# Kernel tuning notes

Hardware: AMD Instinct MI355X
Metric: run time of the kernel (lower is better)

Reference implementation:

```python
import math
import jax, jax.numpy as jnp
import numpy as np

N_HEAD = 12
LN_EPS = 1e-5

def _gelu(x):
    # NewGELU: tanh approximation
    c = math.sqrt(2.0 / math.pi)
    return 0.5 * x * (1.0 + jnp.tanh(c * (x + 0.044715 * x ** 3)))

def _ln(x, w, b):
    m = x.mean(-1, keepdims=True)
    v = x.var(-1, keepdims=True)
    return (x - m) / jnp.sqrt(v + LN_EPS) * w + b

def setup_inputs() -> dict:
    key = jax.random.key(0)
    ks = jax.random.split(key, 8)
    L, C, V, BS = 12, 768, 30522, 1024
    B, T = 4, 1024
    std = 0.02
    inp = {
        'idx': jax.random.randint(ks[0], (B, T), 0, V),
        'wte': jax.random.normal(ks[1], (V, C), jnp.float32) * std,
        'wpe': jax.random.normal(ks[2], (BS, C), jnp.float32) * std,
        'ln1_w': jnp.ones((L, C), jnp.float32),
        'ln1_b': jnp.zeros((L, C), jnp.float32),
        'attn_w': jax.random.normal(ks[3], (L, 3 * C, C), jnp.float32) * std,
        'attn_b': jnp.zeros((L, 3 * C), jnp.float32),
        'proj_w': jax.random.normal(ks[4], (L, C, C), jnp.float32) * (std / math.sqrt(2 * L)),
        'proj_b': jnp.zeros((L, C), jnp.float32),
        'ln2_w': jnp.ones((L, C), jnp.float32),
        'ln2_b': jnp.zeros((L, C), jnp.float32),
        'fc_w': jax.random.normal(ks[5], (L, 4 * C, C), jnp.float32) * std,
        'fc_b': jnp.zeros((L, 4 * C), jnp.float32),
        'mproj_w': jax.random.normal(ks[6], (L, C, 4 * C), jnp.float32) * (std / math.sqrt(2 * L)),
        'mproj_b': jnp.zeros((L, C), jnp.float32),
        'lnf_w': jnp.ones((C,), jnp.float32),
        'lnf_b': jnp.zeros((C,), jnp.float32),
        'lm_head_w': jax.random.normal(ks[7], (V, C), jnp.float32) * std,
    }
    return inp

def reference(idx, wte, wpe, ln1_w, ln1_b, attn_w, attn_b, proj_w, proj_b,
              ln2_w, ln2_b, fc_w, fc_b, mproj_w, mproj_b, lnf_w, lnf_b, lm_head_w):
    B, T = idx.shape
    C = wte.shape[1]
    H = N_HEAD
    D = C // H
    scale = 1.0 / math.sqrt(D)
    x = wte[idx] + wpe[:T][None]  # [B,T,C], drop is identity (p=0)

    def block(x, p):
        l1w, l1b, aw, ab, pw, pb, l2w, l2b, fw, fb, mw, mb = p
        h = _ln(x, l1w, l1b)
        qkv = jnp.einsum('btc,ec->bte', h, aw) + ab  # [B,T,3C]
        q, k, v = jnp.split(qkv, 3, axis=-1)
        q = q.reshape(B, T, H, D)
        k = k.reshape(B, T, H, D)
        v = v.reshape(B, T, H, D)
        att = jnp.einsum('bthd,bshd->bhts', q, k) * scale  # [B,H,T,T]
        att = jax.nn.softmax(att, axis=-1)  # mask=None: full attention
        y = jnp.einsum('bhts,bshd->bthd', att, v).reshape(B, T, C)
        x = x + jnp.einsum('btc,oc->bto', y, pw) + pb
        h = _gelu(jnp.einsum('btc,fc->btf', _ln(x, l2w, l2b), fw) + fb)
        x = x + jnp.einsum('btf,cf->btc', h, mw) + mb
        return x, None

    x, _ = jax.lax.scan(block, x, (ln1_w, ln1_b, attn_w, attn_b, proj_w, proj_b,
                                   ln2_w, ln2_b, fc_w, fc_b, mproj_w, mproj_b))
    x = _ln(x, lnf_w, lnf_b)
    logits = jnp.einsum('btc,vc->btv', x, lm_head_w)  # [B,T,V]
    return logits
```

## Files before the change

### kernel.cpp

```cpp
#include <hip/hip_runtime.h>
#include <hip/hip_bf16.h>
#include <math.h>

typedef __attribute__((ext_vector_type(8))) short short8;
typedef __attribute__((ext_vector_type(4))) float f32x4;

typedef unsigned short u16;

__device__ __forceinline__ u16 f2bf(float f) {
    union { float f; unsigned int u; } v; v.f = f;
    unsigned int u = v.u;
    unsigned int r = (u + 0x7fffu + ((u >> 16) & 1u)) >> 16;
    return (u16)r;
}
__device__ __forceinline__ float bf2f(u16 u) {
    union { unsigned int u; float f; } v; v.u = ((unsigned int)u) << 16;
    return v.f;
}

__device__ __forceinline__ void gload16(const void* g, void* l) {
    __builtin_amdgcn_global_load_lds(
        (const __attribute__((address_space(1))) void*)g,
        (__attribute__((address_space(3))) void*)l, 16, 0, 0);
}

__global__ __launch_bounds__(256) void castw_kernel(const float* __restrict__ src,
                                                    u16* __restrict__ dst,
                                                    long n, long npad) {
    long i = ((long)blockIdx.x * 256 + threadIdx.x) * 4;
    const long stride = (long)gridDim.x * 1024;
    for (; i < npad; i += stride) {
        ushort4 o;
        if (i < n) {
            float4 v = *reinterpret_cast<const float4*>(src + i);
            o.x = f2bf(v.x); o.y = f2bf(v.y); o.z = f2bf(v.z); o.w = f2bf(v.w);
        } else {
            o = make_ushort4(0, 0, 0, 0);
        }
        *reinterpret_cast<ushort4*>(dst + i) = o;
    }
}

__global__ __launch_bounds__(256) void embed_kernel(const int* __restrict__ idx,
                                                    const float* __restrict__ wte,
                                                    const float* __restrict__ wpe,
                                                    float* __restrict__ x) {
    const int row = blockIdx.x;
    const int tid = threadIdx.x;
    const int t = row & 1023;
    const int tok = idx[row];
    const float* we = wte + (size_t)tok * 768;
    const float* pe = wpe + (size_t)t * 768;
    float* xr = x + (size_t)row * 768;
    xr[tid]       = we[tid]       + pe[tid];
    xr[tid + 256] = we[tid + 256] + pe[tid + 256];
    xr[tid + 512] = we[tid + 512] + pe[tid + 512];
}

__global__ __launch_bounds__(256) void ln_kernel(const float* __restrict__ x,
                                                 const float* __restrict__ w,
                                                 const float* __restrict__ b,
                                                 u16* __restrict__ out) {
    const int wid = threadIdx.x >> 6, lane = threadIdx.x & 63;
    const int row = blockIdx.x * 4 + wid;
    const float* xr = x + (size_t)row * 768;
    const float4 v0 = *reinterpret_cast<const float4*>(xr + lane * 4);
    const float4 v1 = *reinterpret_cast<const float4*>(xr + 256 + lane * 4);
    const float4 v2 = *reinterpret_cast<const float4*>(xr + 512 + lane * 4);
    float s = v0.x + v0.y + v0.z + v0.w + v1.x + v1.y + v1.z + v1.w
            + v2.x + v2.y + v2.z + v2.w;
    float q = v0.x * v0.x + v0.y * v0.y + v0.z * v0.z + v0.w * v0.w
            + v1.x * v1.x + v1.y * v1.y + v1.z * v1.z + v1.w * v1.w
            + v2.x * v2.x + v2.y * v2.y + v2.z * v2.z + v2.w * v2.w;
    #pragma unroll
    for (int off = 32; off >= 1; off >>= 1) {
        s += __shfl_xor(s, off);
        q += __shfl_xor(q, off);
    }
    const float mean = s * (1.f / 768.f);
    const float var = q * (1.f / 768.f) - mean * mean;
    const float rstd = rsqrtf(var + 1e-5f);
    u16* orow = out + (size_t)row * 768;
    #pragma unroll
    for (int seg = 0; seg < 3; seg++) {
        const float4 v = seg == 0 ? v0 : (seg == 1 ? v1 : v2);
        const float4 wv = *reinterpret_cast<const float4*>(w + seg * 256 + lane * 4);
        const float4 bv = *reinterpret_cast<const float4*>(b + seg * 256 + lane * 4);
        ushort4 ov;
        ov.x = f2bf((v.x - mean) * rstd * wv.x + bv.x);
        ov.y = f2bf((v.y - mean) * rstd * wv.y + bv.y);
        ov.z = f2bf((v.z - mean) * rstd * wv.z + bv.z);
        ov.w = f2bf((v.w - mean) * rstd * wv.w + bv.w);
        *reinterpret_cast<ushort4*>(orow + seg * 256 + lane * 4) = ov;
    }
}

template<int EPI, int ORDER, int SWZ>
__global__ __launch_bounds__(512) void gemm_big(
        const u16* __restrict__ A, int lda,
        const u16* __restrict__ B, int ldb,
        const float* __restrict__ bias,
        void* __restrict__ Cout, int ldc,
        int N, int K, int nmt) {
    __shared__ __align__(16) u16 lds[2][384 * 32];
    const int tid = threadIdx.x;
    const int lane = tid & 63, wid = tid >> 6;
    const int nwg = gridDim.x;
    const int o = blockIdx.x;
    const int wg = SWZ ? ((o & 7) * (nwg >> 3) + (o >> 3)) : o;
    int m0, n0;
    if (ORDER == 0) { m0 = (wg % nmt) * 256; n0 = (wg / nmt) * 128; }
    else            { n0 = (wg % nmt) * 128; m0 = (wg / nmt) * 256; }

    const int wm = (wid >> 1) * 64, wn = (wid & 1) * 64;
    const int l16 = lane & 15;
    const int qid = lane >> 4;
    const int xq8 = ((qid ^ ((l16 >> 1) & 3)) * 8);

    const int ar = tid >> 2, aq = (tid & 3) ^ ((ar >> 1) & 3);
    const size_t a_src0 = (size_t)(m0 + ar) * lda + aq * 8;
    const size_t a_src1 = (size_t)(m0 + ar + 128) * lda + aq * 8;
    const size_t b_src = (size_t)(n0 + ar) * ldb + aq * 8;

    f32x4 acc[4][4];
    #pragma unroll
    for (int i = 0; i < 4; i++)
        #pragma unroll
        for (int j = 0; j < 4; j++)
            acc[i][j] = (f32x4){0.f, 0.f, 0.f, 0.f};

    const int nk = K >> 5;
    gload16(A + a_src0, lds[0] + tid * 8);
    gload16(A + a_src1, lds[0] + tid * 8 + 4096);
    gload16(B + b_src,  lds[0] + tid * 8 + 8192);

    for (int t = 0; t < nk; ++t) {
        if (t + 1 < nk) {
            u16* buf = lds[(t + 1) & 1];
            const int k0 = (t + 1) << 5;
            gload16(A + a_src0 + k0, buf + tid * 8);
            gload16(A + a_src1 + k0, buf + tid * 8 + 4096);
            gload16(B + b_src + k0,  buf + tid * 8 + 8192);
            asm volatile("s_waitcnt vmcnt(3)" ::: "memory");
        } else {
            asm volatile("s_waitcnt vmcnt(0)" ::: "memory");
        }
        __builtin_amdgcn_s_barrier();
        asm volatile("" ::: "memory");
        const u16* As = lds[t & 1];
        const u16* Bs = lds[t & 1] + 8192;
        short8 af[4], bf[4];
        #pragma unroll
        for (int i = 0; i < 4; i++) {
            af[i] = *reinterpret_cast<const short8*>(&As[(wm + i * 16 + l16) * 32 + xq8]);
            bf[i] = *reinterpret_cast<const short8*>(&Bs[(wn + i * 16 + l16) * 32 + xq8]);
        }
        #pragma unroll
        for (int mi = 0; mi < 4; mi++)
            #pragma unroll
            for (int ni = 0; ni < 4; ni++)
                acc[mi][ni] = __builtin_amdgcn_mfma_f32_16x16x32_bf16(af[mi], bf[ni], acc[mi][ni], 0, 0, 0);
        asm volatile("" ::: "memory");
        __builtin_amdgcn_s_barrier();
    }

    if (EPI == 3) {
        float* ct = reinterpret_cast<float*>(&lds[0][0]) + wid * 1216;
        const int rw = (lane >> 4) * 4;
        const int rr = lane >> 2;
        const int rc = (lane & 3) * 16;
        #pragma unroll
        for (int mi = 0; mi < 4; mi++) {
            asm volatile("" ::: "memory");
            #pragma unroll
            for (int ni = 0; ni < 4; ni++)
                #pragma unroll
                for (int j = 0; j < 4; j++)
                    ct[(rw + j) * 76 + ni * 16 + l16] = acc[mi][ni][j];
            asm volatile("" ::: "memory");
            const int m = m0 + wm + mi * 16 + rr;
            const int nb = n0 + wn + rc;
            float* crow = (float*)Cout + (size_t)m * ldc + nb;
            #pragma unroll
            for (int q = 0; q < 4; q++) {
                const f32x4 v = *reinterpret_cast<const f32x4*>(&ct[rr * 76 + rc + q * 4]);
                if (nb + q * 4 + 3 < N) {
                    *reinterpret_cast<f32x4*>(crow + q * 4) = v;
                } else {
                    #pragma unroll
                    for (int e = 0; e < 4; e++)
                        if (nb + q * 4 + e < N) crow[q * 4 + e] = v[e];
                }
            }
            asm volatile("" ::: "memory");
            __builtin_amdgcn_s_barrier();
        }
    } else {
        const int cb = n0 + wn + l16;
        const int rb = m0 + wm + (lane >> 4) * 4;
        #pragma unroll
        for (int ni = 0; ni < 4; ni++) {
            const int n = cb + ni * 16;
            const float bv = bias[n];
            #pragma unroll
            for (int mi = 0; mi < 4; mi++) {
                #pragma unroll
                for (int j = 0; j < 4; j++) {
                    const int m = rb + mi * 16 + j;
                    float v = acc[mi][ni][j] + bv;
                    if (EPI == 0) {
                        ((u16*)Cout)[(size_t)m * ldc + n] = f2bf(v);
                    } else {
                        const float t = tanhf(0.7978845608028654f * (v + 0.044715f * v * v * v));
                        ((u16*)Cout)[(size_t)m * ldc + n] = f2bf(0.5f * v * (1.f + t));
                    }
                }
            }
        }
    }
}

__global__ __launch_bounds__(256) void gemm_half(
        const u16* __restrict__ A, int lda,
        const u16* __restrict__ B, int ldb,
        const float* __restrict__ bias,
        int ldc, int K, int nmt,
        float* __restrict__ resid) {
    __shared__ __align__(16) u16 lds[2][192 * 32];
    const int tid = threadIdx.x;
    const int lane = tid & 63, wid = tid >> 6;
    const int nwg = gridDim.x;
    const int o = blockIdx.x;
    const int wg = (o & 7) * (nwg >> 3) + (o >> 3);
    const int m0 = (wg % nmt) * 128, n0 = (wg / nmt) * 64;

    const int wm = (wid >> 1) * 64, wn = (wid & 1) * 32;
    const int l16 = lane & 15;
    const int qid = lane >> 4;
    const int xq8 = ((qid ^ ((l16 >> 1) & 3)) * 8);

    const int ar = tid >> 2, aq = (tid & 3) ^ ((ar >> 1) & 3);
    const size_t a_src0 = (size_t)(m0 + ar) * lda + aq * 8;
    const size_t a_src1 = (size_t)(m0 + ar + 64) * lda + aq * 8;
    const size_t b_src = (size_t)(n0 + (tid >> 2)) * ldb + aq * 8;

    f32x4 acc[4][2];
    #pragma unroll
    for (int i = 0; i < 4; i++)
        #pragma unroll
        for (int j = 0; j < 2; j++)
            acc[i][j] = (f32x4){0.f, 0.f, 0.f, 0.f};

    const int nk = K >> 5;
    gload16(A + a_src0, lds[0] + tid * 8);
    gload16(A + a_src1, lds[0] + tid * 8 + 2048);
    gload16(B + b_src,  lds[0] + tid * 8 + 4096);

    for (int t = 0; t < nk; ++t) {
        if (t + 1 < nk) {
            u16* buf = lds[(t + 1) & 1];
            const int k0 = (t + 1) << 5;
            gload16(A + a_src0 + k0, buf + tid * 8);
            gload16(A + a_src1 + k0, buf + tid * 8 + 2048);
            gload16(B + b_src + k0,  buf + tid * 8 + 4096);
            asm volatile("s_waitcnt vmcnt(3)" ::: "memory");
        } else {
            asm volatile("s_waitcnt vmcnt(0)" ::: "memory");
        }
        __builtin_amdgcn_s_barrier();
        asm volatile("" ::: "memory");
        const u16* As = lds[t & 1];
        const u16* Bs = lds[t & 1] + 4096;
        short8 af[4], bf[2];
        #pragma unroll
        for (int i = 0; i < 4; i++)
            af[i] = *reinterpret_cast<const short8*>(&As[(wm + i * 16 + l16) * 32 + xq8]);
        #pragma unroll
        for (int j = 0; j < 2; j++)
            bf[j] = *reinterpret_cast<const short8*>(&Bs[(wn + j * 16 + l16) * 32 + xq8]);
        #pragma unroll
        for (int mi = 0; mi < 4; mi++)
            #pragma unroll
            for (int ni = 0; ni < 2; ni++)
                acc[mi][ni] = __builtin_amdgcn_mfma_f32_16x16x32_bf16(af[mi], bf[ni], acc[mi][ni], 0, 0, 0);
        asm volatile("" ::: "memory");
        __builtin_amdgcn_s_barrier();
    }

    const int cb = n0 + wn + l16;
    const int rb = m0 + wm + (lane >> 4) * 4;
    #pragma unroll
    for (int ni = 0; ni < 2; ni++) {
        const int n = cb + ni * 16;
        const float bv = bias[n];
        #pragma unroll
        for (int mi = 0; mi < 4; mi++) {
            #pragma unroll
            for (int j = 0; j < 4; j++) {
                const int m = rb + mi * 16 + j;
                resid[(size_t)m * ldc + n] += acc[mi][ni][j] + bv;
            }
        }
    }
}

template<int EPI>
__global__ __launch_bounds__(256, 2) void gemm_bt(
        const u16* __restrict__ A, int lda,
        const float* __restrict__ B, int ldb,
        const float* __restrict__ bias,
        void* __restrict__ Cout, int ldc,
        int M, int N, int K,
        float* __restrict__ resid) {
    __shared__ __align__(16) u16 As[128][40];
    __shared__ __align__(16) u16 Bs[128][40];
    const int tid = threadIdx.x;
    const int lane = tid & 63, wid = tid >> 6;
    const int m0 = blockIdx.y * 128, n0 = blockIdx.x * 128;
    const int wm = (wid >> 1) * 64, wn = (wid & 1) * 64;
    const int l16 = lane & 15, lk = (lane >> 4) * 8;

    f32x4 acc[4][4];
    #pragma unroll
    for (int i = 0; i < 4; i++)
        #pragma unroll
        for (int j = 0; j < 4; j++)
            acc[i][j] = (f32x4){0.f, 0.f, 0.f, 0.f};

    for (int k0 = 0; k0 < K; k0 += 32) {
        #pragma unroll
        for (int p = 0; p < 2; p++) {
            const int e = p * 256 + tid;
            const int r = e >> 2, c = e & 3;
            uint4 v = *reinterpret_cast<const uint4*>(A + (size_t)(m0 + r) * lda + k0 + c * 8);
            *reinterpret_cast<uint4*>(&As[r][c * 8]) = v;
        }
        #pragma unroll
        for (int p = 0; p < 4; p++) {
            const int e = p * 256 + tid;
            const int r = e >> 3, c = e & 7;
            float4 v = make_float4(0.f, 0.f, 0.f, 0.f);
            if (n0 + r < N)
                v = *reinterpret_cast<const float4*>(B + (size_t)(n0 + r) * ldb + k0 + c * 4);
            ushort4 hv;
            hv.x = f2bf(v.x); hv.y = f2bf(v.y); hv.z = f2bf(v.z); hv.w = f2bf(v.w);
            *reinterpret_cast<ushort4*>(&Bs[r][c * 4]) = hv;
        }
        __syncthreads();
        short8 af[4], bfr[4];
        #pragma unroll
        for (int i = 0; i < 4; i++) {
            af[i]  = *reinterpret_cast<const short8*>(&As[wm + i * 16 + l16][lk]);
            bfr[i] = *reinterpret_cast<const short8*>(&Bs[wn + i * 16 + l16][lk]);
        }
        #pragma unroll
        for (int mi = 0; mi < 4; mi++)
            #pragma unroll
            for (int ni = 0; ni < 4; ni++)
                acc[mi][ni] = __builtin_amdgcn_mfma_f32_16x16x32_bf16(af[mi], bfr[ni], acc[mi][ni], 0, 0, 0);
        __syncthreads();
    }

    const int cb = n0 + wn + l16;
    const int rb = m0 + wm + (lane >> 4) * 4;
    #pragma unroll
    for (int ni = 0; ni < 4; ni++) {
        const int n = cb + ni * 16;
        if (n >= N) continue;
        float bv = 0.f;
        if (EPI != 3) bv = bias[n];
        #pragma unroll
        for (int mi = 0; mi < 4; mi++) {
            #pragma unroll
            for (int j = 0; j < 4; j++) {
                const int m = rb + mi * 16 + j;
                float v = acc[mi][ni][j] + bv;
                if (EPI == 0) {
                    ((u16*)Cout)[(size_t)m * ldc + n] = f2bf(v);
                } else if (EPI == 1) {
                    resid[(size_t)m * ldc + n] += v;
                } else if (EPI == 2) {
                    const float t = tanhf(0.7978845608028654f * (v + 0.044715f * v * v * v));
                    ((u16*)Cout)[(size_t)m * ldc + n] = f2bf(0.5f * v * (1.f + t));
                } else {
                    ((float*)Cout)[(size_t)m * ldc + n] = v;
                }
            }
        }
    }
}

__global__ __launch_bounds__(512, 2) void attn_mfma_kernel(const u16* __restrict__ qkv,
                                                           u16* __restrict__ y) {
    __shared__ __align__(16) u16 Qs[128][72];
    __shared__ __align__(16) u16 Ks[2][64][72];
    __shared__ __align__(16) u16 Vt[2][64][72];
    __shared__ __align__(16) u16 Ps[8][16][72];

    const int tid = threadIdx.x;
    const int lane = tid & 63, wid = tid >> 6;
    const int l16 = lane & 15, lk = (lane >> 4) * 8;
    const int qt = blockIdx.x, h = blockIdx.y, b = blockIdx.z;

    const size_t base = (size_t)b * 1024 * 2304;
    const u16* qp = qkv + base + (size_t)(qt * 128) * 2304 + h * 64;
    const u16* kp = qkv + base + 768  + h * 64;
    const u16* vp = qkv + base + 1536 + h * 64;

    const int krr = tid >> 3, kc8 = tid & 7;
    const int vs = (tid >> 4) * 2, vdq = tid & 15;

    #pragma unroll
    for (int p = 0; p < 2; p++) {
        const int e = p * 512 + tid;
        const int rr = e >> 3, c8 = e & 7;
        *reinterpret_cast<uint4*>(&Qs[rr][c8 * 8]) =
            *reinterpret_cast<const uint4*>(qp + (size_t)rr * 2304 + c8 * 8);
    }
    uint4 kreg; ushort4 vra, vrb;
    kreg = *reinterpret_cast<const uint4*>(kp + (size_t)krr * 2304 + kc8 * 8);
    vra = *reinterpret_cast<const ushort4*>(vp + (size_t)vs * 2304 + vdq * 4);
    vrb = *reinterpret_cast<const ushort4*>(vp + (size_t)(vs + 1) * 2304 + vdq * 4);
    __syncthreads();

    short8 qf[2];
    #pragma unroll
    for (int kk = 0; kk < 2; kk++)
        qf[kk] = *reinterpret_cast<const short8*>(&Qs[wid * 16 + l16][kk * 32 + lk]);

    *reinterpret_cast<uint4*>(&Ks[0][krr][kc8 * 8]) = kreg;
    *reinterpret_cast<ushort2*>(&Vt[0][vdq * 4 + 0][vs]) = make_ushort2(vra.x, vrb.x);
    *reinterpret_cast<ushort2*>(&Vt[0][vdq * 4 + 1][vs]) = make_ushort2(vra.y, vrb.y);
    *reinterpret_cast<ushort2*>(&Vt[0][vdq * 4 + 2][vs]) = make_ushort2(vra.z, vrb.z);
    *reinterpret_cast<ushort2*>(&Vt[0][vdq * 4 + 3][vs]) = make_ushort2(vra.w, vrb.w);
    __syncthreads();

    f32x4 o_acc[4];
    #pragma unroll
    for (int i = 0; i < 4; i++) o_acc[i] = (f32x4){0.f, 0.f, 0.f, 0.f};
    float l_part[4] = {0.f, 0.f, 0.f, 0.f};

    for (int t = 0; t < 16; ++t) {
        const int cur = t & 1, nxt = cur ^ 1;
        if (t + 1 < 16) {
            const int s0 = (t + 1) * 64;
            kreg = *reinterpret_cast<const uint4*>(kp + (size_t)(s0 + krr) * 2304 + kc8 * 8);
            vra = *reinterpret_cast<const ushort4*>(vp + (size_t)(s0 + vs) * 2304 + vdq * 4);
            vrb = *reinterpret_cast<const ushort4*>(vp + (size_t)(s0 + vs + 1) * 2304 + vdq * 4);
        }

        f32x4 sa[4];
        #pragma unroll
        for (int i = 0; i < 4; i++) sa[i] = (f32x4){0.f, 0.f, 0.f, 0.f};
        #pragma unroll
        for (int nj = 0; nj < 4; nj++) {
            #pragma unroll
            for (int kk = 0; kk < 2; kk++) {
                short8 kf = *reinterpret_cast<const short8*>(&Ks[cur][nj * 16 + l16][kk * 32 + lk]);
                sa[nj] = __builtin_amdgcn_mfma_f32_16x16x32_bf16(qf[kk], kf, sa[nj], 0, 0, 0);
            }
        }
        #pragma unroll
        for (int nj = 0; nj < 4; nj++) {
            #pragma unroll
            for (int r = 0; r < 4; r++) {
                const float pv = __expf(sa[nj][r] * 0.125f);
                l_part[r] += pv;
                Ps[wid][(lane >> 4) * 4 + r][nj * 16 + l16] = f2bf(pv);
            }
        }
        short8 pa[2];
        #pragma unroll
        for (int kk = 0; kk < 2; kk++)
            pa[kk] = *reinterpret_cast<const short8*>(&Ps[wid][l16][kk * 32 + lk]);
        #pragma unroll
        for (int nd = 0; nd < 4; nd++) {
            #pragma unroll
            for (int kk = 0; kk < 2; kk++) {
                short8 vf = *reinterpret_cast<const short8*>(&Vt[cur][nd * 16 + l16][kk * 32 + lk]);
                o_acc[nd] = __builtin_amdgcn_mfma_f32_16x16x32_bf16(pa[kk], vf, o_acc[nd], 0, 0, 0);
            }
        }

        if (t + 1 < 16) {
            *reinterpret_cast<uint4*>(&Ks[nxt][krr][kc8 * 8]) = kreg;
            *reinterpret_cast<ushort2*>(&Vt[nxt][vdq * 4 + 0][vs]) = make_ushort2(vra.x, vrb.x);
            *reinterpret_cast<ushort2*>(&Vt[nxt][vdq * 4 + 1][vs]) = make_ushort2(vra.y, vrb.y);
            *reinterpret_cast<ushort2*>(&Vt[nxt][vdq * 4 + 2][vs]) = make_ushort2(vra.z, vrb.z);
            *reinterpret_cast<ushort2*>(&Vt[nxt][vdq * 4 + 3][vs]) = make_ushort2(vra.w, vrb.w);
        }
        __syncthreads();
    }

    float inv[4];
    #pragma unroll
    for (int r = 0; r < 4; r++) {
        float s = l_part[r];
        #pragma unroll
        for (int off = 8; off >= 1; off >>= 1) s += __shfl_xor(s, off);
        inv[r] = 1.f / s;
    }
    const int rowb = b * 1024 + qt * 128 + wid * 16 + (lane >> 4) * 4;
    #pragma unroll
    for (int nd = 0; nd < 4; nd++) {
        const int col = h * 64 + nd * 16 + l16;
        #pragma unroll
        for (int r = 0; r < 4; r++) {
            y[(size_t)(rowb + r) * 768 + col] = f2bf(o_acc[nd][r] * inv[r]);
        }
    }
}

extern "C" void kernel_launch(void* const* d_in, const int* in_sizes, int n_in,
                              void* d_out, int out_size, void* d_ws, size_t ws_size,
                              hipStream_t stream) {
    (void)in_sizes; (void)n_in; (void)out_size;
    const int*   idx    = (const int*)d_in[0];
    const float* wte    = (const float*)d_in[1];
    const float* wpe    = (const float*)d_in[2];
    const float* ln1w   = (const float*)d_in[3];
    const float* ln1b   = (const float*)d_in[4];
    const float* attnw  = (const float*)d_in[5];
    const float* attnb  = (const float*)d_in[6];
    const float* projw  = (const float*)d_in[7];
    const float* projb  = (const float*)d_in[8];
    const float* ln2w   = (const float*)d_in[9];
    const float* ln2b   = (const float*)d_in[10];
    const float* fcw    = (const float*)d_in[11];
    const float* fcb    = (const float*)d_in[12];
    const float* mprojw = (const float*)d_in[13];
    const float* mprojb = (const float*)d_in[14];
    const float* lnfw   = (const float*)d_in[15];
    const float* lnfb   = (const float*)d_in[16];
    const float* lmw    = (const float*)d_in[17];
    float* out = (float*)d_out;

    char* p = (char*)d_ws;
    size_t used = 0;
    auto take = [&](size_t bytes) { char* q = p + used; used += (bytes + 255) & ~(size_t)255; return q; };
    float* x      = (float*)take((size_t)4096 * 768 * 4);
    u16*   a_bf   = (u16*)take((size_t)4096 * 768 * 2);
    u16*   qkv_bf = (u16*)take((size_t)4096 * 2304 * 2);
    u16*   hid_bf = (u16*)take((size_t)4096 * 3072 * 2);
    u16*   w_lm   = (u16*)take((size_t)30592 * 768 * 2);
    const bool castLm = used <= ws_size;
    u16*   w_attn = (u16*)take((size_t)12 * 2304 * 768 * 2);
    u16*   w_proj = (u16*)take((size_t)12 * 768 * 768 * 2);
    u16*   w_fc   = (u16*)take((size_t)12 * 3072 * 768 * 2);
    u16*   w_mprj = (u16*)take((size_t)12 * 768 * 3072 * 2);
    const bool castAll = used <= ws_size;

    embed_kernel<<<4096, 256, 0, stream>>>(idx, wte, wpe, x);

    if (castLm)
        castw_kernel<<<2048, 256, 0, stream>>>(lmw, w_lm, (long)30522 * 768, (long)30592 * 768);
    if (castAll) {
        castw_kernel<<<2048, 256, 0, stream>>>(attnw,  w_attn, (long)12 * 2304 * 768, (long)12 * 2304 * 768);
        castw_kernel<<<2048, 256, 0, stream>>>(projw,  w_proj, (long)12 * 768 * 768,  (long)12 * 768 * 768);
        castw_kernel<<<2048, 256, 0, stream>>>(fcw,    w_fc,   (long)12 * 3072 * 768, (long)12 * 3072 * 768);
        castw_kernel<<<2048, 256, 0, stream>>>(mprojw, w_mprj, (long)12 * 768 * 3072, (long)12 * 768 * 3072);
    }

    for (int l = 0; l < 12; l++) {
        ln_kernel<<<1024, 256, 0, stream>>>(x, ln1w + l * 768, ln1b + l * 768, a_bf);
        if (castAll) {
            gemm_big<0, 0, 1><<<16 * 18, 512, 0, stream>>>(
                a_bf, 768, w_attn + (size_t)l * 2304 * 768, 768, attnb + l * 2304,
                (void*)qkv_bf, 2304, 2304, 768, 16);
        } else {
            gemm_bt<0><<<dim3(18, 32), 256, 0, stream>>>(
                a_bf, 768, attnw + (size_t)l * 2304 * 768, 768, attnb + l * 2304,
                (void*)qkv_bf, 2304, 4096, 2304, 768, nullptr);
        }
        attn_mfma_kernel<<<dim3(8, 12, 4), 512, 0, stream>>>(qkv_bf, a_bf);
        if (castAll) {
            gemm_half<<<32 * 12, 256, 0, stream>>>(
                a_bf, 768, w_proj + (size_t)l * 768 * 768, 768, projb + l * 768,
                768, 768, 32, x);
        } else {
            gemm_bt<1><<<dim3(6, 32), 256, 0, stream>>>(
                a_bf, 768, projw + (size_t)l * 768 * 768, 768, projb + l * 768,
                nullptr, 768, 4096, 768, 768, x);
        }
        ln_kernel<<<1024, 256, 0, stream>>>(x, ln2w + l * 768, ln2b + l * 768, a_bf);
        if (castAll) {
            gemm_big<2, 0, 1><<<16 * 24, 512, 0, stream>>>(
                a_bf, 768, w_fc + (size_t)l * 3072 * 768, 768, fcb + l * 3072,
                (void*)hid_bf, 3072, 3072, 768, 16);
            gemm_half<<<32 * 12, 256, 0, stream>>>(
                hid_bf, 3072, w_mprj + (size_t)l * 768 * 3072, 3072, mprojb + l * 768,
                768, 3072, 32, x);
        } else {
            gemm_bt<2><<<dim3(24, 32), 256, 0, stream>>>(
                a_bf, 768, fcw + (size_t)l * 3072 * 768, 768, fcb + l * 3072,
                (void*)hid_bf, 3072, 4096, 3072, 768, nullptr);
            gemm_bt<1><<<dim3(6, 32), 256, 0, stream>>>(
                hid_bf, 3072, mprojw + (size_t)l * 768 * 3072, 3072, mprojb + l * 768,
                nullptr, 768, 4096, 768, 3072, x);
        }
    }

    ln_kernel<<<1024, 256, 0, stream>>>(x, lnfw, lnfb, a_bf);
    if (castLm) {
        gemm_big<3, 0, 0><<<16 * 239, 512, 0, stream>>>(
            a_bf, 768, w_lm, 768, nullptr, (void*)out, 30522, 30522, 768, 16);
    } else {
        gemm_bt<3><<<dim3(239, 32), 256, 0, stream>>>(
            a_bf, 768, lmw, 768, nullptr, (void*)out, 30522, 4096, 30522, 768, nullptr);
    }
}
```

Measured before the change: 2.723 ms.

## Use dedicated 256x256-tile GEMM kernel for the LM head projection

Measured after the change: 2.735 ms. About the same (+0.5%).

```diff
diff --git a/kernel.cpp b/kernel.cpp
--- a/kernel.cpp
+++ b/kernel.cpp
@@ -95,7 +95,7 @@
     }
 }
 
-template<int EPI, int ORDER, int SWZ>
+template<int EPI>
 __global__ __launch_bounds__(512) void gemm_big(
         const u16* __restrict__ A, int lda,
         const u16* __restrict__ B, int ldb,
@@ -107,10 +107,8 @@
     const int lane = tid & 63, wid = tid >> 6;
     const int nwg = gridDim.x;
     const int o = blockIdx.x;
-    const int wg = SWZ ? ((o & 7) * (nwg >> 3) + (o >> 3)) : o;
-    int m0, n0;
-    if (ORDER == 0) { m0 = (wg % nmt) * 256; n0 = (wg / nmt) * 128; }
-    else            { n0 = (wg % nmt) * 128; m0 = (wg / nmt) * 256; }
+    const int wg = (o & 7) * (nwg >> 3) + (o >> 3);
+    const int m0 = (wg % nmt) * 256, n0 = (wg / nmt) * 128;
 
     const int wm = (wid >> 1) * 64, wn = (wid & 1) * 64;
     const int l16 = lane & 15;
@@ -164,26 +162,117 @@
         __builtin_amdgcn_s_barrier();
     }
 
-    if (EPI == 3) {
-        float* ct = reinterpret_cast<float*>(&lds[0][0]) + wid * 1216;
-        const int rw = (lane >> 4) * 4;
-        const int rr = lane >> 2;
-        const int rc = (lane & 3) * 16;
+    const int cb = n0 + wn + l16;
+    const int rb = m0 + wm + (lane >> 4) * 4;
+    #pragma unroll
+    for (int ni = 0; ni < 4; ni++) {
+        const int n = cb + ni * 16;
+        const float bv = bias[n];
         #pragma unroll
         for (int mi = 0; mi < 4; mi++) {
+            #pragma unroll
+            for (int j = 0; j < 4; j++) {
+                const int m = rb + mi * 16 + j;
+                float v = acc[mi][ni][j] + bv;
+                if (EPI == 0) {
+                    ((u16*)Cout)[(size_t)m * ldc + n] = f2bf(v);
+                } else {
+                    const float t = tanhf(0.7978845608028654f * (v + 0.044715f * v * v * v));
+                    ((u16*)Cout)[(size_t)m * ldc + n] = f2bf(0.5f * v * (1.f + t));
+                }
+            }
+        }
+    }
+}
+
+__global__ __launch_bounds__(512) void gemm_256(
+        const u16* __restrict__ A, int lda,
+        const u16* __restrict__ B, int ldb,
+        void* __restrict__ Cout, int ldc,
+        int N, int K, int nmt) {
+    __shared__ __align__(16) u16 lds[2][512 * 32];
+    const int tid = threadIdx.x;
+    const int lane = tid & 63, wid = tid >> 6;
+    const int wg = blockIdx.x;
+    const int m0 = (wg % nmt) * 256, n0 = (wg / nmt) * 256;
+
+    const int wm = (wid >> 1) * 64, wn = (wid & 1) * 128;
+    const int l16 = lane & 15;
+    const int qid = lane >> 4;
+    const int xq8 = ((qid ^ ((l16 >> 1) & 3)) * 8);
+
+    const int ar = tid >> 2, aq = (tid & 3) ^ ((ar >> 1) & 3);
+    const size_t a_src0 = (size_t)(m0 + ar) * lda + aq * 8;
+    const size_t a_src1 = (size_t)(m0 + ar + 128) * lda + aq * 8;
+    const size_t b_src0 = (size_t)(n0 + ar) * ldb + aq * 8;
+    const size_t b_src1 = (size_t)(n0 + ar + 128) * ldb + aq * 8;
+
+    f32x4 acc[4][8];
+    #pragma unroll
+    for (int i = 0; i < 4; i++)
+        #pragma unroll
+        for (int j = 0; j < 8; j++)
+            acc[i][j] = (f32x4){0.f, 0.f, 0.f, 0.f};
+
+    const int nk = K >> 5;
+    gload16(A + a_src0, lds[0] + tid * 8);
+    gload16(A + a_src1, lds[0] + tid * 8 + 4096);
+    gload16(B + b_src0, lds[0] + tid * 8 + 8192);
+    gload16(B + b_src1, lds[0] + tid * 8 + 12288);
+
+    for (int t = 0; t < nk; ++t) {
+        if (t + 1 < nk) {
+            u16* buf = lds[(t + 1) & 1];
+            const int k0 = (t + 1) << 5;
+            gload16(A + a_src0 + k0, buf + tid * 8);
+            gload16(A + a_src1 + k0, buf + tid * 8 + 4096);
+            gload16(B + b_src0 + k0, buf + tid * 8 + 8192);
+            gload16(B + b_src1 + k0, buf + tid * 8 + 12288);
+            asm volatile("s_waitcnt vmcnt(4)" ::: "memory");
+        } else {
+            asm volatile("s_waitcnt vmcnt(0)" ::: "memory");
+        }
+        __builtin_amdgcn_s_barrier();
+        asm volatile("" ::: "memory");
+        const u16* As = lds[t & 1];
+        const u16* Bs = lds[t & 1] + 8192;
+        short8 af[4], bf[8];
+        #pragma unroll
+        for (int i = 0; i < 4; i++)
+            af[i] = *reinterpret_cast<const short8*>(&As[(wm + i * 16 + l16) * 32 + xq8]);
+        #pragma unroll
+        for (int j = 0; j < 8; j++)
+            bf[j] = *reinterpret_cast<const short8*>(&Bs[(wn + j * 16 + l16) * 32 + xq8]);
+        #pragma unroll
+        for (int mi = 0; mi < 4; mi++)
+            #pragma unroll
+            for (int ni = 0; ni < 8; ni++)
+                acc[mi][ni] = __builtin_amdgcn_mfma_f32_16x16x32_bf16(af[mi], bf[ni], acc[mi][ni], 0, 0, 0);
+        asm volatile("" ::: "memory");
+        __builtin_amdgcn_s_barrier();
+    }
+
+    float* ct = reinterpret_cast<float*>(&lds[0][0]) + wid * 1088;
+    const int rw = (lane >> 4) * 4;
+    const int rr = lane >> 2;
+    const int rc = (lane & 3) * 16;
+    #pragma unroll
+    for (int mi = 0; mi < 4; mi++) {
+        #pragma unroll
+        for (int hn = 0; hn < 2; hn++) {
             asm volatile("" ::: "memory");
             #pragma unroll
-            for (int ni = 0; ni < 4; ni++)
+            for (int q = 0; q < 4; q++)
                 #pragma unroll
                 for (int j = 0; j < 4; j++)
-                    ct[(rw + j) * 76 + ni * 16 + l16] = acc[mi][ni][j];
+                    ct[(rw + j) * 68 + q * 16 + l16] = acc[mi][hn * 4 + q][j];
             asm volatile("" ::: "memory");
             const int m = m0 + wm + mi * 16 + rr;
-            const int nb = n0 + wn + rc;
+            const int nb = n0 + wn + hn * 64 + rc;
             float* crow = (float*)Cout + (size_t)m * ldc + nb;
             #pragma unroll
             for (int q = 0; q < 4; q++) {
-                const f32x4 v = *reinterpret_cast<const f32x4*>(&ct[rr * 76 + rc + q * 4]);
+                const f32x4 v = *reinterpret_cast<const f32x4*>(&ct[rr * 68 + rc + q * 4]);
                 if (nb + q * 4 + 3 < N) {
                     *reinterpret_cast<f32x4*>(crow + q * 4) = v;
                 } else {
@@ -193,29 +282,6 @@
                 }
             }
             asm volatile("" ::: "memory");
-            __builtin_amdgcn_s_barrier();
-        }
-    } else {
-        const int cb = n0 + wn + l16;
-        const int rb = m0 + wm + (lane >> 4) * 4;
-        #pragma unroll
-        for (int ni = 0; ni < 4; ni++) {
-            const int n = cb + ni * 16;
-            const float bv = bias[n];
-            #pragma unroll
-            for (int mi = 0; mi < 4; mi++) {
-                #pragma unroll
-                for (int j = 0; j < 4; j++) {
-                    const int m = rb + mi * 16 + j;
-                    float v = acc[mi][ni][j] + bv;
-                    if (EPI == 0) {
-                        ((u16*)Cout)[(size_t)m * ldc + n] = f2bf(v);
-                    } else {
-                        const float t = tanhf(0.7978845608028654f * (v + 0.044715f * v * v * v));
-                        ((u16*)Cout)[(size_t)m * ldc + n] = f2bf(0.5f * v * (1.f + t));
-                    }
-                }
-            }
         }
     }
 }
@@ -542,7 +608,7 @@
     u16*   a_bf   = (u16*)take((size_t)4096 * 768 * 2);
     u16*   qkv_bf = (u16*)take((size_t)4096 * 2304 * 2);
     u16*   hid_bf = (u16*)take((size_t)4096 * 3072 * 2);
-    u16*   w_lm   = (u16*)take((size_t)30592 * 768 * 2);
+    u16*   w_lm   = (u16*)take((size_t)30720 * 768 * 2);
     const bool castLm = used <= ws_size;
     u16*   w_attn = (u16*)take((size_t)12 * 2304 * 768 * 2);
     u16*   w_proj = (u16*)take((size_t)12 * 768 * 768 * 2);
@@ -553,7 +619,7 @@
     embed_kernel<<<4096, 256, 0, stream>>>(idx, wte, wpe, x);
 
     if (castLm)
-        castw_kernel<<<2048, 256, 0, stream>>>(lmw, w_lm, (long)30522 * 768, (long)30592 * 768);
+        castw_kernel<<<2048, 256, 0, stream>>>(lmw, w_lm, (long)30522 * 768, (long)30720 * 768);
     if (castAll) {
         castw_kernel<<<2048, 256, 0, stream>>>(attnw,  w_attn, (long)12 * 2304 * 768, (long)12 * 2304 * 768);
         castw_kernel<<<2048, 256, 0, stream>>>(projw,  w_proj, (long)12 * 768 * 768,  (long)12 * 768 * 768);
@@ -564,7 +630,7 @@
     for (int l = 0; l < 12; l++) {
         ln_kernel<<<1024, 256, 0, stream>>>(x, ln1w + l * 768, ln1b + l * 768, a_bf);
         if (castAll) {
-            gemm_big<0, 0, 1><<<16 * 18, 512, 0, stream>>>(
+            gemm_big<0><<<16 * 18, 512, 0, stream>>>(
                 a_bf, 768, w_attn + (size_t)l * 2304 * 768, 768, attnb + l * 2304,
                 (void*)qkv_bf, 2304, 2304, 768, 16);
         } else {
@@ -584,7 +650,7 @@
         }
         ln_kernel<<<1024, 256, 0, stream>>>(x, ln2w + l * 768, ln2b + l * 768, a_bf);
         if (castAll) {
-            gemm_big<2, 0, 1><<<16 * 24, 512, 0, stream>>>(
+            gemm_big<2><<<16 * 24, 512, 0, stream>>>(
                 a_bf, 768, w_fc + (size_t)l * 3072 * 768, 768, fcb + l * 3072,
                 (void*)hid_bf, 3072, 3072, 768, 16);
             gemm_half<<<32 * 12, 256, 0, stream>>>(
@@ -602,8 +668,8 @@
 
     ln_kernel<<<1024, 256, 0, stream>>>(x, lnfw, lnfb, a_bf);
     if (castLm) {
-        gemm_big<3, 0, 0><<<16 * 239, 512, 0, stream>>>(
-            a_bf, 768, w_lm, 768, nullptr, (void*)out, 30522, 30522, 768, 16);
+        gemm_256<<<16 * 120, 512, 0, stream>>>(
+            a_bf, 768, w_lm, 768, (void*)out, 30522, 30522, 768, 16);
     } else {
         gemm_bt<3><<<dim3(239, 32), 256, 0, stream>>>(
             a_bf, 768, lmw, 768, nullptr, (void*)out, 30522, 4096, 30522, 768, nullptr);
```
